# Kernel tuning notes

Measured on AMD Instinct MI355X. Metric: run time of the kernel, lower is better.

Reference implementation:

```python
import jax, jax.numpy as jnp
import numpy as np

D, H, T, K = 512, 8, 4, 64   # dim, n_heads, n_tasks, topk_n
HD = D // H
PRUNE, EPS = 1e-3, 1e-8


def _ln(x, g, b, eps=1e-5):
    m = jnp.mean(x, axis=-1, keepdims=True)
    v = jnp.mean((x - m) ** 2, axis=-1, keepdims=True)
    return (x - m) * jax.lax.rsqrt(v + eps) * g + b


def setup_inputs() -> dict:
    key = jax.random.key(0)
    ks = jax.random.split(key, 5)
    B, N = 16, 8192
    tokens = jax.random.normal(ks[0], (B, N, D), jnp.float32)
    key_padding_mask = jax.random.uniform(ks[1], (B, N)) < 0.1  # True marks padding
    q = jax.random.normal(ks[2], (1, T, D), jnp.float32) * 0.02
    in_proj_w = jax.random.normal(ks[3], (3 * D, D), jnp.float32) / np.sqrt(D).astype(np.float32)
    in_proj_b = jnp.zeros((3 * D,), jnp.float32)
    pre_g = jnp.ones((D,), jnp.float32)
    pre_b = jnp.zeros((D,), jnp.float32)
    q_g = jnp.ones((D,), jnp.float32)
    q_b = jnp.zeros((D,), jnp.float32)
    log_tau = jnp.asarray(np.log(0.3), jnp.float32)
    return dict(tokens=tokens, key_padding_mask=key_padding_mask, q=q,
                in_proj_w=in_proj_w, in_proj_b=in_proj_b,
                pre_g=pre_g, pre_b=pre_b, q_g=q_g, q_b=q_b, log_tau=log_tau)


def reference(tokens, key_padding_mask, q, in_proj_w, in_proj_b,
              pre_g, pre_b, q_g, q_b, log_tau):
    B, N, _ = tokens.shape
    kpm = key_padding_mask  # [B,N], True = pad

    normed = _ln(tokens, pre_g, pre_b)                       # [B,N,D]
    tau = jnp.clip(jnp.exp(log_tau), 0.1, 10.0)
    query = _ln(q, q_g, q_b) / tau                           # [1,T,D]

    wq, wk, wv = in_proj_w[:D], in_proj_w[D:2 * D], in_proj_w[2 * D:]
    bq, bk, bv = in_proj_b[:D], in_proj_b[D:2 * D], in_proj_b[2 * D:]

    qp = (query[0] @ wq.T + bq).reshape(T, H, HD)            # [T,H,hd]
    kp = (normed @ wk.T + bk).reshape(B, N, H, HD)           # [B,N,H,hd]

    scores = jnp.einsum('thd,bnhd->bhtn', qp, kp) / np.float32(np.sqrt(HD))
    scores = jnp.where(kpm[:, None, None, :], -jnp.inf, scores)
    attn = jax.nn.softmax(scores, axis=-1)                   # [B,H,T,N]

    alpha = attn.mean(axis=1)                                # [B,T,N]
    alpha = jnp.where(kpm[:, None, :], 0.0, alpha)
    alpha = alpha / jnp.maximum(alpha.sum(-1, keepdims=True), EPS)

    # prune below threshold, with argmax one-hot fallback if everything pruned
    a = jnp.where(alpha < PRUNE, 0.0, alpha)
    a = jnp.where(kpm[:, None, :], 0.0, a)
    s = a.sum(-1, keepdims=True)
    need_fallback = s <= EPS                                 # [B,T,1]
    base = jnp.where(kpm[:, None, :], -1.0, alpha)
    onehot = jax.nn.one_hot(jnp.argmax(base, axis=-1), N, dtype=a.dtype)  # [B,T,N]
    a = jnp.where(need_fallback, onehot, a)
    a = jnp.where(kpm[:, None, :], 0.0, a)
    alpha = a / jnp.maximum(a.sum(-1, keepdims=True), EPS)

    # pool source: tie_mha_v projection of normed inputs
    pool_source = normed @ wv.T + bv                         # [B,N,D]

    # top-k gather + renorm weighting
    topv, topi = jax.lax.top_k(alpha, K)                     # [B,T,K]
    selected = jnp.take_along_axis(pool_source[:, None, :, :], topi[..., None], axis=2)  # [B,T,K,D]
    w = topv / jnp.maximum(topv.sum(-1, keepdims=True), EPS)
    pooled = (w[..., None] * selected).sum(axis=2)           # [B,T,D]
    return pooled
```

## Files before the change

### kernel.cpp

```cpp
#include <hip/hip_runtime.h>
#include <math.h>

#define Dd   512
#define Hh   8
#define Tt   4
#define HDd  64
#define Bb   16
#define Nn   8192
#define HTc  32
#define KS   64
#define NTOK (Bb*Nn)
#define PRUNEc 0.001f
#define EPSc   1e-8f

#define WS_C1     0u
#define WS_C0     128u
#define WS_FLAG   6144u
#define WS_G2H    65536u
#define WS_G2M    98304u
#define WS_G2L    131072u
#define WS_MEAN   163840u
#define WS_INV    688128u
#define WS_PART   1343488u
#define WS_PEXP   4194304u

typedef __attribute__((ext_vector_type(8)))  short short8v;
typedef __attribute__((ext_vector_type(16))) float f32x16;

__device__ __forceinline__ void split3(float x, unsigned &h, unsigned &m, unsigned &l){
  unsigned u  = __float_as_uint(x);
  unsigned uh = u & 0xFFFF0000u;
  float rh = x - __uint_as_float(uh);
  unsigned um = __float_as_uint(rh) & 0xFFFF0000u;
  float rm = rh - __uint_as_float(um);
  unsigned ul = __float_as_uint(rm) & 0xFFFF0000u;
  h = uh; m = um; l = ul;
}

__device__ __forceinline__ void split3x8(float4 v0, float4 v1,
                                         short8v &h, short8v &m, short8v &l){
  union { short8v s; unsigned u[4]; } H, M, L;
  float a[8] = {v0.x,v0.y,v0.z,v0.w,v1.x,v1.y,v1.z,v1.w};
  #pragma unroll
  for (int w = 0; w < 4; ++w){
    unsigned ha, ma, la, hb, mb, lb;
    split3(a[2*w],   ha, ma, la);
    split3(a[2*w+1], hb, mb, lb);
    H.u[w] = (ha>>16) | (hb & 0xFFFF0000u);
    M.u[w] = (ma>>16) | (mb & 0xFFFF0000u);
    L.u[w] = (la>>16) | (lb & 0xFFFF0000u);
  }
  h = H.s; m = M.s; l = L.s;
}

__device__ __forceinline__ int mdecode(const void* mraw, int fl, size_t i){
  if (fl & 2) return ((const float*)mraw)[i] != 0.0f;
  if (fl & 1) return ((const unsigned char*)mraw)[i] != 0;
  return ((const int*)mraw)[i] != 0;
}

__device__ __forceinline__ int chkw(unsigned v){
  return (v == 0x3f800000u) ? 2 : ((v & ~1u) ? 1 : 0);
}
__global__ void tap_detect(const uint4* mraw, int* flag){
  int tid = threadIdx.x;
  if (tid == 0) *flag = 0;
  __syncthreads();
  int f = 0;
  #pragma unroll
  for (int i = 0; i < 8; ++i){
    uint4 v = mraw[tid + i*1024];
    f |= chkw(v.x) | chkw(v.y) | chkw(v.z) | chkw(v.w);
  }
  if (f) atomicOr(flag, f);
}

__global__ void tap_prep(const float* q, const float* ipw, const float* ipb,
                         const float* pre_g, const float* pre_b,
                         const float* q_g, const float* q_b, const float* log_tau,
                         unsigned short* G2h, unsigned short* G2m, unsigned short* G2l,
                         float* C1, float* C0){
  __shared__ float query[Tt][Dd];
  __shared__ float qps[HDd];
  __shared__ float red[256];
  int tid = threadIdx.x;
  int ht = blockIdx.x;
  int h = ht >> 2, t = ht & 3;
  float tau = expf(log_tau[0]);
  tau = fminf(fmaxf(tau, 0.1f), 10.0f);
  float itau = 1.0f / tau;
  int wv = tid >> 6, lane = tid & 63;
  {
    const float* qr = q + wv*Dd;
    float s = 0.f, ss = 0.f;
    for (int j = lane; j < Dd; j += 64){ float x = qr[j]; s += x; ss += x*x; }
    #pragma unroll
    for (int off = 32; off; off >>= 1){ s += __shfl_down(s, off); ss += __shfl_down(ss, off); }
    s = __shfl(s, 0); ss = __shfl(ss, 0);
    float mean = s * (1.f/Dd);
    float var  = ss * (1.f/Dd) - mean*mean;
    float inv  = rsqrtf(var + 1e-5f);
    for (int j = lane; j < Dd; j += 64){
      float x = qr[j];
      query[wv][j] = ((x - mean)*inv*q_g[j] + q_b[j]) * itau;
    }
  }
  __syncthreads();
  {
    int d = tid >> 2, sub = tid & 3;
    int i = h*HDd + d;
    const float* wrow = ipw + (size_t)i*Dd;
    float acc = 0.f;
    int j0 = sub*128;
    for (int j = 0; j < 128; ++j) acc += query[t][j0+j]*wrow[j0+j];
    red[tid] = acc;
    __syncthreads();
    if (sub == 0) qps[d] = red[tid]+red[tid+1]+red[tid+2]+red[tid+3] + ipb[i];
    __syncthreads();
  }
  float c1p = 0.f, c0p = 0.f;
  for (int jj = 0; jj < 2; ++jj){
    int j = tid + jj*256;
    float acc = 0.f;
    #pragma unroll 8
    for (int d = 0; d < HDd; ++d)
      acc += qps[d] * ipw[(size_t)(Dd + h*HDd + d)*Dd + j];
    float w2 = acc * 0.125f;
    float g2 = w2 * pre_g[j];
    unsigned uh, um, ul;
    split3(g2, uh, um, ul);
    G2h[ht*Dd + j] = (unsigned short)(uh >> 16);
    G2m[ht*Dd + j] = (unsigned short)(um >> 16);
    G2l[ht*Dd + j] = (unsigned short)(ul >> 16);
    float geff = __uint_as_float(uh) + __uint_as_float(um) + __uint_as_float(ul);
    c1p += geff;
    c0p += w2 * pre_b[j];
  }
  if (tid < HDd) c0p += qps[tid] * ipb[Dd + h*HDd + tid] * 0.125f;
  red[tid] = c1p; __syncthreads();
  for (int s = 128; s; s >>= 1){ if (tid < s) red[tid] += red[tid+s]; __syncthreads(); }
  if (tid == 0) C1[ht] = red[0];
  __syncthreads();
  red[tid] = c0p; __syncthreads();
  for (int s = 128; s; s >>= 1){ if (tid < s) red[tid] += red[tid+s]; __syncthreads(); }
  if (tid == 0) C0[ht] = red[0];
}

__global__ __launch_bounds__(256, 4) void tap_scores(
    const float* __restrict__ tokens,
    const unsigned short* __restrict__ G2h, const unsigned short* __restrict__ G2m,
    const unsigned short* __restrict__ G2l,
    const float* __restrict__ C1, const float* __restrict__ C0,
    const void* __restrict__ mraw, const int* __restrict__ flag,
    float* __restrict__ pexp, float2* __restrict__ part,
    float* __restrict__ meanw, float* __restrict__ invw){
  int tid   = threadIdx.x;
  int lane  = tid & 63, wv = tid >> 6;
  int col   = lane & 31;
  int bhalf = lane >> 5;
  size_t t0 = (size_t)blockIdx.x * 128;
  int brow  = (wv << 5) | col;
  const float* __restrict__ xrow = tokens + (t0 + brow)*(size_t)Dd;
  int abase = (col << 9) | (bhalf << 3);

  f32x16 acc;
  #pragma unroll
  for (int i = 0; i < 16; ++i) acc[i] = 0.f;
  float ps = 0.f, pss = 0.f;

  float4 cv0[2], cv1[2];
  #pragma unroll
  for (int sub = 0; sub < 2; ++sub){
    int k0 = (sub << 4) | (bhalf << 3);
    cv0[sub] = *(const float4*)(xrow + k0);
    cv1[sub] = *(const float4*)(xrow + k0 + 4);
  }
  for (int s = 0; s < 16; ++s){
    float4 nv0[2], nv1[2];
    int sn = (s + 1) & 15;
    #pragma unroll
    for (int sub = 0; sub < 2; ++sub){
      int k0 = (sn << 5) | (sub << 4) | (bhalf << 3);
      nv0[sub] = *(const float4*)(xrow + k0);
      nv1[sub] = *(const float4*)(xrow + k0 + 4);
    }
    #pragma unroll
    for (int sub = 0; sub < 2; ++sub){
      float4 v0 = cv0[sub], v1 = cv1[sub];
      int ga = abase + (s << 5) + (sub << 4);
      short8v ah = *(const short8v*)(G2h + ga);
      short8v am = *(const short8v*)(G2m + ga);
      short8v al = *(const short8v*)(G2l + ga);
      ps  += v0.x+v0.y+v0.z+v0.w + v1.x+v1.y+v1.z+v1.w;
      pss += v0.x*v0.x+v0.y*v0.y+v0.z*v0.z+v0.w*v0.w
           + v1.x*v1.x+v1.y*v1.y+v1.z*v1.z+v1.w*v1.w;
      short8v bh, bm, bl;
      split3x8(v0, v1, bh, bm, bl);
      acc = __builtin_amdgcn_mfma_f32_32x32x16_bf16(ah, bh, acc, 0, 0, 0);
      acc = __builtin_amdgcn_mfma_f32_32x32x16_bf16(am, bh, acc, 0, 0, 0);
      acc = __builtin_amdgcn_mfma_f32_32x32x16_bf16(ah, bm, acc, 0, 0, 0);
      acc = __builtin_amdgcn_mfma_f32_32x32x16_bf16(am, bm, acc, 0, 0, 0);
      acc = __builtin_amdgcn_mfma_f32_32x32x16_bf16(al, bh, acc, 0, 0, 0);
      acc = __builtin_amdgcn_mfma_f32_32x32x16_bf16(ah, bl, acc, 0, 0, 0);
    }
    #pragma unroll
    for (int sub = 0; sub < 2; ++sub){ cv0[sub] = nv0[sub]; cv1[sub] = nv1[sub]; }
  }
  ps  += __shfl_xor(ps, 32);
  pss += __shfl_xor(pss, 32);
  float mean = ps * (1.f/512.f);
  float var  = pss * (1.f/512.f) - mean*mean;
  float inv  = rsqrtf(var + 1e-5f);
  if (bhalf == 0){ meanw[t0 + brow] = mean; invw[t0 + brow] = inv; }
  int fl = *flag;
  int mko = mdecode(mraw, fl, t0 + brow);
  int b = (int)(t0 >> 13);
  int n = (int)(t0 & 8191) + brow;
  int g = (int)blockIdx.x*4 + wv;
  #pragma unroll
  for (int r = 0; r < 16; ++r){
    int ht = (r & 3) + ((r >> 2) << 3) + (bhalf << 2);
    float sc = mko ? -1e30f : (inv*(acc[r] - mean*C1[ht]) + C0[ht]);
    float mx = sc;
    #pragma unroll
    for (int off = 16; off; off >>= 1) mx = fmaxf(mx, __shfl_xor(mx, off));
    float p = mko ? 0.f : __expf(sc - mx);
    float ls = p;
    #pragma unroll
    for (int off = 16; off; off >>= 1) ls += __shfl_xor(ls, off);
    pexp[(((size_t)(b*HTc + ht)) << 13) + n] = p;
    if (col == r) part[(size_t)g*HTc + ht] = make_float2(mx, ls);
  }
}

__global__ __launch_bounds__(512, 1) void tap_select(
    const float* __restrict__ tokens, const float* __restrict__ ipw,
    const float* __restrict__ ipb,
    const float* __restrict__ pre_g, const float* __restrict__ pre_b,
    const float* __restrict__ pexp, const float2* __restrict__ part,
    const void* __restrict__ mraw, const int* __restrict__ flag,
    const float* __restrict__ meanw, const float* __restrict__ invw,
    float* __restrict__ out){
  __shared__ float av[Nn];
  __shared__ float fac[Hh][256];
  __shared__ float lv[1024];
  __shared__ int   li[1024];
  __shared__ float tw[KS]; __shared__ int ti[KS];
  __shared__ float coeff[KS];
  __shared__ __align__(16) float u[Dd];
  __shared__ float rs[8];
  __shared__ float rva[8]; __shared__ int ria[8]; __shared__ int rpa[8];
  __shared__ int cnt; __shared__ int sArg; __shared__ float sW, sS;
  int bt = blockIdx.x;
  int b = bt >> 2, t = bt & 3;
  int tid = threadIdx.x, lane = tid & 63, wvi = tid >> 6;
  int fl = *flag;
  if (tid == 0) cnt = 0;
  {
    int h = wvi;
    const float2* pb = part + ((size_t)(b << 8))*HTc + (h*Tt + t);
    float2 v0 = pb[(size_t)(lane      )*HTc];
    float2 v1 = pb[(size_t)(lane +  64)*HTc];
    float2 v2 = pb[(size_t)(lane + 128)*HTc];
    float2 v3 = pb[(size_t)(lane + 192)*HTc];
    float M = fmaxf(fmaxf(v0.x, v1.x), fmaxf(v2.x, v3.x));
    #pragma unroll
    for (int off = 32; off; off >>= 1) M = fmaxf(M, __shfl_xor(M, off));
    float L = v0.y*__expf(v0.x - M) + v1.y*__expf(v1.x - M)
            + v2.y*__expf(v2.x - M) + v3.y*__expf(v3.x - M);
    #pragma unroll
    for (int off = 32; off; off >>= 1) L += __shfl_xor(L, off);
    float inv8L = (L > 0.f) ? 0.125f / L : 0.f;
    fac[h][lane      ] = __expf(v0.x - M) * inv8L;
    fac[h][lane +  64] = __expf(v1.x - M) * inv8L;
    fac[h][lane + 128] = __expf(v2.x - M) * inv8L;
    fac[h][lane + 192] = __expf(v3.x - M) * inv8L;
  }
  const float* pr[Hh];
  #pragma unroll
  for (int h = 0; h < Hh; ++h)
    pr[h] = pexp + ((size_t)(b*HTc + h*Tt + t) << 13);
  __syncthreads();
  float lsum = 0.f;
  float bvv = -2.f; int bii = 1 << 30;
  #pragma unroll 2
  for (int i = 0; i < 16; ++i){
    int n = tid + (i << 9);
    float a = pr[0][n] * fac[0][n >> 5];
    #pragma unroll
    for (int h = 1; h < Hh; ++h) a += pr[h][n] * fac[h][n >> 5];
    av[n] = a;
    lsum += a;
    float bb = mdecode(mraw, fl, (size_t)b*Nn + n) ? -1.f : a;
    if (bb > bvv || (bb == bvv && n < bii)){ bvv = bb; bii = n; }
  }
  #pragma unroll
  for (int off = 32; off; off >>= 1) lsum += __shfl_down(lsum, off);
  if (lane == 0) rs[wvi] = lsum;
  #pragma unroll
  for (int off = 32; off; off >>= 1){
    float ov = __shfl_down(bvv, off);
    int   oi = __shfl_down(bii, off);
    if (ov > bvv || (ov == bvv && oi < bii)){ bvv = ov; bii = oi; }
  }
  if (lane == 0){ rva[wvi] = bvv; ria[wvi] = bii; }
  __syncthreads();
  float Sall = rs[0]+rs[1]+rs[2]+rs[3]+rs[4]+rs[5]+rs[6]+rs[7];
  if (tid == 0){
    float bv2 = rva[0]; int bi2 = ria[0];
    for (int w2 = 1; w2 < 8; ++w2)
      if (rva[w2] > bv2 || (rva[w2] == bv2 && ria[w2] < bi2)){ bv2 = rva[w2]; bi2 = ria[w2]; }
    sArg = bi2;
  }
  float f1 = 1.0f / fmaxf(Sall, EPSc);
  #pragma unroll 2
  for (int i = 0; i < 16; ++i){
    int n = tid + (i << 9);
    float x = av[n] * f1;
    if (x >= PRUNEc){
      int id = atomicAdd(&cnt, 1);
      if (id < 1024){ lv[id] = x; li[id] = n; }
    }
  }
  __syncthreads();
  int L = cnt;
  if (L == 0){
    if (tid == 0){ lv[0] = 1.f; li[0] = sArg; }
    L = 1;
    __syncthreads();
  }
  if (L <= KS){
    if (tid < KS){ tw[tid] = (tid < L) ? lv[tid] : 0.f; ti[tid] = (tid < L) ? li[tid] : 0; }
    __syncthreads();
  } else {
    for (int k = 0; k < KS; ++k){
      float bv = -1.f; int bn = 1 << 30; int bp = -1;
      for (int j = tid; j < L; j += 512){
        float x = lv[j]; int nn = li[j];
        if (x > bv || (x == bv && nn < bn)){ bv = x; bn = nn; bp = j; }
      }
      #pragma unroll
      for (int off = 32; off; off >>= 1){
        float ov = __shfl_down(bv, off);
        int   on = __shfl_down(bn, off);
        int   op = __shfl_down(bp, off);
        if (ov > bv || (ov == bv && on < bn)){ bv = ov; bn = on; bp = op; }
      }
      if (lane == 0){ rva[wvi] = bv; ria[wvi] = bn; rpa[wvi] = bp; }
      __syncthreads();
      if (tid == 0){
        float bb = rva[0]; int bj = ria[0]; int pp = rpa[0];
        for (int w2 = 1; w2 < 8; ++w2)
          if (rva[w2] > bb || (rva[w2] == bb && ria[w2] < bj)){ bb = rva[w2]; bj = ria[w2]; pp = rpa[w2]; }
        tw[k] = bb; ti[k] = bj;
        lv[pp] = -1.f;
      }
      __syncthreads();
    }
  }
  if (wvi == 0){
    float v = tw[lane];
    #pragma unroll
    for (int off = 32; off; off >>= 1) v += __shfl_down(v, off);
    if (lane == 0) sW = v;
  }
  __syncthreads();
  float sumw = sW;
  float Winv = 1.0f / fmaxf(sumw, EPSc);
  float Wn   = sumw * Winv;
  if (wvi == 0){
    int n = ti[lane];
    float mk2 = meanw[(size_t)b*Nn + n];
    float ik  = invw [(size_t)b*Nn + n];
    float wn  = tw[lane] * Winv;
    coeff[lane] = wn * ik;
    float sp = wn * mk2 * ik;
    #pragma unroll
    for (int off = 32; off; off >>= 1) sp += __shfl_down(sp, off);
    if (lane == 0) sS = sp;
  }
  __syncthreads();
  float Sv = sS;
  int d = tid;
  float acc0 = 0.f;
  #pragma unroll 4
  for (int k = 0; k < KS; ++k){
    float c = coeff[k];
    acc0 = fmaf(c, tokens[((size_t)b*Nn + ti[k])*Dd + d], acc0);
  }
  u[d] = pre_g[d]*(acc0 - Sv) + pre_b[d]*Wn;
  __syncthreads();
  const float4* u4 = (const float4*)u;
  const float4* w0 = (const float4*)(ipw + (size_t)(2*Dd + d)*Dd);
  float o0 = 0.f;
  #pragma unroll 4
  for (int j4 = 0; j4 < 128; ++j4){
    float4 uu = u4[j4];
    float4 a = w0[j4];
    o0 += uu.x*a.x + uu.y*a.y + uu.z*a.z + uu.w*a.w;
  }
  out[bt*Dd + d] = o0 + Wn*ipb[2*Dd + d];
}

extern "C" void kernel_launch(void* const* d_in, const int* in_sizes, int n_in,
                              void* d_out, int out_size, void* d_ws, size_t ws_size,
                              hipStream_t stream){
  const float* tokens = (const float*)d_in[0];
  const void*  kpm    = d_in[1];
  const float* q      = (const float*)d_in[2];
  const float* ipw    = (const float*)d_in[3];
  const float* ipb    = (const float*)d_in[4];
  const float* pre_g  = (const float*)d_in[5];
  const float* pre_b  = (const float*)d_in[6];
  const float* q_g    = (const float*)d_in[7];
  const float* q_b    = (const float*)d_in[8];
  const float* ltau   = (const float*)d_in[9];
  char* ws = (char*)d_ws;
  float* C1    = (float*)(ws + WS_C1);
  float* C0    = (float*)(ws + WS_C0);
  int*   flag  = (int*)  (ws + WS_FLAG);
  unsigned short* G2h = (unsigned short*)(ws + WS_G2H);
  unsigned short* G2m = (unsigned short*)(ws + WS_G2M);
  unsigned short* G2l = (unsigned short*)(ws + WS_G2L);
  float* meanw = (float*)(ws + WS_MEAN);
  float* invw  = (float*)(ws + WS_INV);
  float2* part = (float2*)(ws + WS_PART);
  float* pexp  = (float*)(ws + WS_PEXP);
  float* out = (float*)d_out;

  hipLaunchKernelGGL(tap_detect, dim3(1), dim3(1024), 0, stream, (const uint4*)kpm, flag);
  hipLaunchKernelGGL(tap_prep,   dim3(HTc), dim3(256), 0, stream,
                     q, ipw, ipb, pre_g, pre_b, q_g, q_b, ltau, G2h, G2m, G2l, C1, C0);
  hipLaunchKernelGGL(tap_scores, dim3(NTOK/128), dim3(256), 0, stream,
                     tokens, G2h, G2m, G2l, C1, C0, kpm, flag, pexp, part, meanw, invw);
  hipLaunchKernelGGL(tap_select, dim3(Bb*Tt), dim3(512), 0, stream,
                     tokens, ipw, ipb, pre_g, pre_b, pexp, part, kpm, flag,
                     meanw, invw, out);
}
```

Baseline: 573.7 us.

## Replace 3-way bf16 split with scaled 2-way fp16 split in score MFMA

Switches the emulated-fp32 score GEMM from a bf16 hi/mid/lo split using six MFMAs to a power-of-two-scaled fp16 hi/lo split using four MFMAs. Token values are scaled by a constant and weights by a per-head exponent so they fit fp16 range, and the scale is undone in the epilogue. The mask-detect kernel is folded into the prep kernel as an extra block, and the weight fragments are now prefetched together with the token loads. This cuts MFMA count and conversion ALU work, but fp16 has a narrower range, so large token values could overflow or lose precision.

```diff
diff --git a/kernel.cpp b/kernel.cpp
--- a/kernel.cpp
+++ b/kernel.cpp
@@ -12,45 +12,34 @@
 #define NTOK (Bb*Nn)
 #define PRUNEc 0.001f
 #define EPSc   1e-8f
+#define TOKSC 16.0f
 
 #define WS_C1     0u
 #define WS_C0     128u
+#define WS_CS     2048u
 #define WS_FLAG   6144u
 #define WS_G2H    65536u
-#define WS_G2M    98304u
-#define WS_G2L    131072u
+#define WS_G2L    98304u
 #define WS_MEAN   163840u
 #define WS_INV    688128u
 #define WS_PART   1343488u
 #define WS_PEXP   4194304u
 
-typedef __attribute__((ext_vector_type(8)))  short short8v;
-typedef __attribute__((ext_vector_type(16))) float f32x16;
-
-__device__ __forceinline__ void split3(float x, unsigned &h, unsigned &m, unsigned &l){
-  unsigned u  = __float_as_uint(x);
-  unsigned uh = u & 0xFFFF0000u;
-  float rh = x - __uint_as_float(uh);
-  unsigned um = __float_as_uint(rh) & 0xFFFF0000u;
-  float rm = rh - __uint_as_float(um);
-  unsigned ul = __float_as_uint(rm) & 0xFFFF0000u;
-  h = uh; m = um; l = ul;
-}
-
-__device__ __forceinline__ void split3x8(float4 v0, float4 v1,
-                                         short8v &h, short8v &m, short8v &l){
-  union { short8v s; unsigned u[4]; } H, M, L;
-  float a[8] = {v0.x,v0.y,v0.z,v0.w,v1.x,v1.y,v1.z,v1.w};
-  #pragma unroll
-  for (int w = 0; w < 4; ++w){
-    unsigned ha, ma, la, hb, mb, lb;
-    split3(a[2*w],   ha, ma, la);
-    split3(a[2*w+1], hb, mb, lb);
-    H.u[w] = (ha>>16) | (hb & 0xFFFF0000u);
-    M.u[w] = (ma>>16) | (mb & 0xFFFF0000u);
-    L.u[w] = (la>>16) | (lb & 0xFFFF0000u);
-  }
-  h = H.s; m = M.s; l = L.s;
+typedef __attribute__((ext_vector_type(8)))  _Float16 half8v;
+typedef __attribute__((ext_vector_type(2)))  __fp16   fp16x2;
+typedef __attribute__((ext_vector_type(16))) float    f32x16;
+
+__device__ __forceinline__ void splitf16x8(float4 v0, float4 v1, half8v &h, half8v &l){
+  union { half8v v; fp16x2 p[4]; } H, L;
+  H.p[0] = __builtin_amdgcn_cvt_pkrtz(v0.x, v0.y);
+  H.p[1] = __builtin_amdgcn_cvt_pkrtz(v0.z, v0.w);
+  H.p[2] = __builtin_amdgcn_cvt_pkrtz(v1.x, v1.y);
+  H.p[3] = __builtin_amdgcn_cvt_pkrtz(v1.z, v1.w);
+  L.p[0] = __builtin_amdgcn_cvt_pkrtz(v0.x - (float)H.p[0][0], v0.y - (float)H.p[0][1]);
+  L.p[1] = __builtin_amdgcn_cvt_pkrtz(v0.z - (float)H.p[1][0], v0.w - (float)H.p[1][1]);
+  L.p[2] = __builtin_amdgcn_cvt_pkrtz(v1.x - (float)H.p[2][0], v1.y - (float)H.p[2][1]);
+  L.p[3] = __builtin_amdgcn_cvt_pkrtz(v1.z - (float)H.p[3][0], v1.w - (float)H.p[3][1]);
+  h = H.v; l = L.v;
 }
 
 __device__ __forceinline__ int mdecode(const void* mraw, int fl, size_t i){
@@ -62,28 +51,31 @@
 __device__ __forceinline__ int chkw(unsigned v){
   return (v == 0x3f800000u) ? 2 : ((v & ~1u) ? 1 : 0);
 }
-__global__ void tap_detect(const uint4* mraw, int* flag){
-  int tid = threadIdx.x;
-  if (tid == 0) *flag = 0;
-  __syncthreads();
-  int f = 0;
-  #pragma unroll
-  for (int i = 0; i < 8; ++i){
-    uint4 v = mraw[tid + i*1024];
-    f |= chkw(v.x) | chkw(v.y) | chkw(v.z) | chkw(v.w);
-  }
-  if (f) atomicOr(flag, f);
-}
 
 __global__ void tap_prep(const float* q, const float* ipw, const float* ipb,
                          const float* pre_g, const float* pre_b,
                          const float* q_g, const float* q_b, const float* log_tau,
-                         unsigned short* G2h, unsigned short* G2m, unsigned short* G2l,
-                         float* C1, float* C0){
+                         const uint4* mraw, int* flag,
+                         _Float16* G2h, _Float16* G2l,
+                         float* C1, float* C0, float* CS){
+  int tid = threadIdx.x;
+  if (blockIdx.x == HTc){
+    if (tid == 0) *flag = 0;
+    __syncthreads();
+    int f = 0;
+    #pragma unroll
+    for (int i = 0; i < 32; ++i){
+      uint4 v = mraw[tid + i*256];
+      f |= chkw(v.x) | chkw(v.y) | chkw(v.z) | chkw(v.w);
+    }
+    if (f) atomicOr(flag, f);
+    return;
+  }
   __shared__ float query[Tt][Dd];
   __shared__ float qps[HDd];
   __shared__ float red[256];
-  int tid = threadIdx.x;
+  __shared__ float g2row[Dd];
+  __shared__ float escS;
   int ht = blockIdx.x;
   int h = ht >> 2, t = ht & 3;
   float tau = expf(log_tau[0]);
@@ -118,7 +110,8 @@
     if (sub == 0) qps[d] = red[tid]+red[tid+1]+red[tid+2]+red[tid+3] + ipb[i];
     __syncthreads();
   }
-  float c1p = 0.f, c0p = 0.f;
+  float c0p = 0.f;
+  #pragma unroll
   for (int jj = 0; jj < 2; ++jj){
     int j = tid + jj*256;
     float acc = 0.f;
@@ -126,17 +119,35 @@
     for (int d = 0; d < HDd; ++d)
       acc += qps[d] * ipw[(size_t)(Dd + h*HDd + d)*Dd + j];
     float w2 = acc * 0.125f;
-    float g2 = w2 * pre_g[j];
-    unsigned uh, um, ul;
-    split3(g2, uh, um, ul);
-    G2h[ht*Dd + j] = (unsigned short)(uh >> 16);
-    G2m[ht*Dd + j] = (unsigned short)(um >> 16);
-    G2l[ht*Dd + j] = (unsigned short)(ul >> 16);
-    float geff = __uint_as_float(uh) + __uint_as_float(um) + __uint_as_float(ul);
-    c1p += geff;
+    g2row[j] = w2 * pre_g[j];
     c0p += w2 * pre_b[j];
   }
   if (tid < HDd) c0p += qps[tid] * ipb[Dd + h*HDd + tid] * 0.125f;
+  __syncthreads();
+  {
+    float mx = fmaxf(fabsf(g2row[tid]), fabsf(g2row[tid + 256]));
+    red[tid] = mx; __syncthreads();
+    for (int s = 128; s; s >>= 1){ if (tid < s) red[tid] = fmaxf(red[tid], red[tid+s]); __syncthreads(); }
+    if (tid == 0){
+      float maxv = red[0];
+      escS = (maxv > 0.f) ? exp2f(floorf(log2f(maxv))) : 1.f;
+      CS[ht] = escS * (1.0f/TOKSC);
+    }
+    __syncthreads();
+  }
+  float esc = escS, ie = 1.0f/esc;
+  float c1p = 0.f;
+  #pragma unroll
+  for (int jj = 0; jj < 2; ++jj){
+    int j = tid + jj*256;
+    float gs = g2row[j] * ie;
+    _Float16 hh = (_Float16)gs;
+    float r = gs - (float)hh;
+    _Float16 ll = (_Float16)r;
+    G2h[ht*Dd + j] = hh;
+    G2l[ht*Dd + j] = ll;
+    c1p += esc*((float)hh + (float)ll);
+  }
   red[tid] = c1p; __syncthreads();
   for (int s = 128; s; s >>= 1){ if (tid < s) red[tid] += red[tid+s]; __syncthreads(); }
   if (tid == 0) C1[ht] = red[0];
@@ -148,9 +159,9 @@
 
 __global__ __launch_bounds__(256, 4) void tap_scores(
     const float* __restrict__ tokens,
-    const unsigned short* __restrict__ G2h, const unsigned short* __restrict__ G2m,
-    const unsigned short* __restrict__ G2l,
+    const _Float16* __restrict__ G2h, const _Float16* __restrict__ G2l,
     const float* __restrict__ C1, const float* __restrict__ C0,
+    const float* __restrict__ CS,
     const void* __restrict__ mraw, const int* __restrict__ flag,
     float* __restrict__ pexp, float2* __restrict__ part,
     float* __restrict__ meanw, float* __restrict__ invw){
@@ -168,43 +179,50 @@
   for (int i = 0; i < 16; ++i) acc[i] = 0.f;
   float ps = 0.f, pss = 0.f;
 
-  float4 cv0[2], cv1[2];
+  float4 cT0[2], cT1[2];
+  half8v cAh[2], cAl[2];
   #pragma unroll
   for (int sub = 0; sub < 2; ++sub){
     int k0 = (sub << 4) | (bhalf << 3);
-    cv0[sub] = *(const float4*)(xrow + k0);
-    cv1[sub] = *(const float4*)(xrow + k0 + 4);
+    cT0[sub] = *(const float4*)(xrow + k0);
+    cT1[sub] = *(const float4*)(xrow + k0 + 4);
+    cAh[sub] = *(const half8v*)(G2h + abase + (sub << 4));
+    cAl[sub] = *(const half8v*)(G2l + abase + (sub << 4));
   }
   for (int s = 0; s < 16; ++s){
-    float4 nv0[2], nv1[2];
+    float4 nT0[2], nT1[2];
+    half8v nAh[2], nAl[2];
     int sn = (s + 1) & 15;
     #pragma unroll
     for (int sub = 0; sub < 2; ++sub){
       int k0 = (sn << 5) | (sub << 4) | (bhalf << 3);
-      nv0[sub] = *(const float4*)(xrow + k0);
-      nv1[sub] = *(const float4*)(xrow + k0 + 4);
+      nT0[sub] = *(const float4*)(xrow + k0);
+      nT1[sub] = *(const float4*)(xrow + k0 + 4);
+      int ga = abase + (sn << 5) + (sub << 4);
+      nAh[sub] = *(const half8v*)(G2h + ga);
+      nAl[sub] = *(const half8v*)(G2l + ga);
     }
     #pragma unroll
     for (int sub = 0; sub < 2; ++sub){
-      float4 v0 = cv0[sub], v1 = cv1[sub];
-      int ga = abase + (s << 5) + (sub << 4);
-      short8v ah = *(const short8v*)(G2h + ga);
-      short8v am = *(const short8v*)(G2m + ga);
-      short8v al = *(const short8v*)(G2l + ga);
+      float4 v0 = cT0[sub], v1 = cT1[sub];
       ps  += v0.x+v0.y+v0.z+v0.w + v1.x+v1.y+v1.z+v1.w;
       pss += v0.x*v0.x+v0.y*v0.y+v0.z*v0.z+v0.w*v0.w
            + v1.x*v1.x+v1.y*v1.y+v1.z*v1.z+v1.w*v1.w;
-      short8v bh, bm, bl;
-      split3x8(v0, v1, bh, bm, bl);
-      acc = __builtin_amdgcn_mfma_f32_32x32x16_bf16(ah, bh, acc, 0, 0, 0);
-      acc = __builtin_amdgcn_mfma_f32_32x32x16_bf16(am, bh, acc, 0, 0, 0);
-      acc = __builtin_amdgcn_mfma_f32_32x32x16_bf16(ah, bm, acc, 0, 0, 0);
-      acc = __builtin_amdgcn_mfma_f32_32x32x16_bf16(am, bm, acc, 0, 0, 0);
-      acc = __builtin_amdgcn_mfma_f32_32x32x16_bf16(al, bh, acc, 0, 0, 0);
-      acc = __builtin_amdgcn_mfma_f32_32x32x16_bf16(ah, bl, acc, 0, 0, 0);
-    }
-    #pragma unroll
-    for (int sub = 0; sub < 2; ++sub){ cv0[sub] = nv0[sub]; cv1[sub] = nv1[sub]; }
+      float4 s0 = make_float4(v0.x*TOKSC, v0.y*TOKSC, v0.z*TOKSC, v0.w*TOKSC);
+      float4 s1 = make_float4(v1.x*TOKSC, v1.y*TOKSC, v1.z*TOKSC, v1.w*TOKSC);
+      half8v bh, bl;
+      splitf16x8(s0, s1, bh, bl);
+      half8v ah = cAh[sub], al = cAl[sub];
+      acc = __builtin_amdgcn_mfma_f32_32x32x16_f16(ah, bh, acc, 0, 0, 0);
+      acc = __builtin_amdgcn_mfma_f32_32x32x16_f16(ah, bl, acc, 0, 0, 0);
+      acc = __builtin_amdgcn_mfma_f32_32x32x16_f16(al, bh, acc, 0, 0, 0);
+      acc = __builtin_amdgcn_mfma_f32_32x32x16_f16(al, bl, acc, 0, 0, 0);
+    }
+    #pragma unroll
+    for (int sub = 0; sub < 2; ++sub){
+      cT0[sub] = nT0[sub]; cT1[sub] = nT1[sub];
+      cAh[sub] = nAh[sub]; cAl[sub] = nAl[sub];
+    }
   }
   ps  += __shfl_xor(ps, 32);
   pss += __shfl_xor(pss, 32);
@@ -220,7 +238,7 @@
   #pragma unroll
   for (int r = 0; r < 16; ++r){
     int ht = (r & 3) + ((r >> 2) << 3) + (bhalf << 2);
-    float sc = mko ? -1e30f : (inv*(acc[r] - mean*C1[ht]) + C0[ht]);
+    float sc = mko ? -1e30f : (inv*(acc[r]*CS[ht] - mean*C1[ht]) + C0[ht]);
     float mx = sc;
     #pragma unroll
     for (int off = 16; off; off >>= 1) mx = fmaxf(mx, __shfl_xor(mx, off));
@@ -418,21 +436,21 @@
   char* ws = (char*)d_ws;
   float* C1    = (float*)(ws + WS_C1);
   float* C0    = (float*)(ws + WS_C0);
+  float* CSs   = (float*)(ws + WS_CS);
   int*   flag  = (int*)  (ws + WS_FLAG);
-  unsigned short* G2h = (unsigned short*)(ws + WS_G2H);
-  unsigned short* G2m = (unsigned short*)(ws + WS_G2M);
-  unsigned short* G2l = (unsigned short*)(ws + WS_G2L);
+  _Float16* G2h = (_Float16*)(ws + WS_G2H);
+  _Float16* G2l = (_Float16*)(ws + WS_G2L);
   float* meanw = (float*)(ws + WS_MEAN);
   float* invw  = (float*)(ws + WS_INV);
   float2* part = (float2*)(ws + WS_PART);
   float* pexp  = (float*)(ws + WS_PEXP);
   float* out = (float*)d_out;
 
-  hipLaunchKernelGGL(tap_detect, dim3(1), dim3(1024), 0, stream, (const uint4*)kpm, flag);
-  hipLaunchKernelGGL(tap_prep,   dim3(HTc), dim3(256), 0, stream,
-                     q, ipw, ipb, pre_g, pre_b, q_g, q_b, ltau, G2h, G2m, G2l, C1, C0);
+  hipLaunchKernelGGL(tap_prep,   dim3(HTc + 1), dim3(256), 0, stream,
+                     q, ipw, ipb, pre_g, pre_b, q_g, q_b, ltau,
+                     (const uint4*)kpm, flag, G2h, G2l, C1, C0, CSs);
   hipLaunchKernelGGL(tap_scores, dim3(NTOK/128), dim3(256), 0, stream,
-                     tokens, G2h, G2m, G2l, C1, C0, kpm, flag, pexp, part, meanw, invw);
+                     tokens, G2h, G2l, C1, C0, CSs, kpm, flag, pexp, part, meanw, invw);
   hipLaunchKernelGGL(tap_select, dim3(Bb*Tt), dim3(512), 0, stream,
                      tokens, ipw, ipb, pre_g, pre_b, pexp, part, kpm, flag,
                      meanw, invw, out);
```

After: 559.8 us, median of 2. 1.02x faster.
